# Kernel tuning notes

Measured on AMD Instinct MI355X. Metric: run time of the kernel, lower is better.

The kernel has to match this reference:

```python
import jax, jax.numpy as jnp
import numpy as np

H = 64      # hidden_dimension
NH = 4      # num_heads
L = 2       # num_egat_layers
N = 20000   # total nodes in batched graph
E = 320000  # total edges
B = 64      # number of graphs in batch
SLOPE = 0.2 # DGL EGATConv leaky_relu negative slope


def setup_inputs() -> dict:
    key = jax.random.key(0)
    ks = iter(jax.random.split(key, 40))
    def nrm(shape, scale=0.05):
        return jax.random.normal(next(ks), shape, dtype=jnp.float32) * scale
    node_graph_id = jnp.sort(jax.random.randint(next(ks), (N,), 0, B))
    src = jax.random.randint(next(ks), (E,), 0, N)
    dst = jax.random.randint(next(ks), (E,), 0, N)
    edge_graph_id = node_graph_id[dst]
    return dict(
        x=nrm((N, 81), 1.0), e=nrm((E, 17), 1.0),
        placed_rc=jax.random.randint(next(ks), (N,), 0, 2),
        fp=nrm((B, 2048), 1.0),
        src=src, dst=dst, node_graph_id=node_graph_id, edge_graph_id=edge_graph_id,
        W_fp=nrm((2048, H)), b_fp=jnp.zeros((H,), jnp.float32),
        W_n0=nrm((81, H)), b_n0=jnp.zeros((H,), jnp.float32),
        W_e0=nrm((17, H)), b_e0=jnp.zeros((H,), jnp.float32),
        emb_rc=nrm((2, H)),
        fc_node_W=nrm((L, H, NH * H)), fc_ni_W=nrm((L, H, NH * H)),
        fc_nj_W=nrm((L, H, NH * H)), fc_fij_W=nrm((L, H, NH * H)),
        attn=nrm((L, NH, H)), egat_bias=jnp.zeros((L, NH * H), jnp.float32),
        mlp_n_W=nrm((L, NH * H, H)), mlp_n_b=jnp.zeros((L, H), jnp.float32),
        mlp_e_W=nrm((L, NH * H, H)), mlp_e_b=jnp.zeros((L, H), jnp.float32),
        W_g=nrm((3 * H, H)), b_g=jnp.zeros((H,), jnp.float32),
    )


def _egat_layer(nf, ef, src, dst, p):
    # One EGATLayer: DGL EGATConv + per-output MLP + ELU.
    fcnW, fniW, fnjW, ffW, attn, ebias, mnW, mnb, meW, meb = p
    f_out = nf[src] @ fniW + nf[dst] @ fnjW + ef @ ffW          # [E, NH*H]
    f_out = jax.nn.leaky_relu(f_out, SLOPE).reshape(E, NH, H)    # [E, NH, H]
    logits = jnp.einsum('ehd,hd->eh', f_out, attn)               # [E, NH]
    # edge softmax over incoming edges at each destination node
    m = jax.ops.segment_max(logits, dst, num_segments=N)
    ex = jnp.exp(logits - m[dst])
    denom = jax.ops.segment_sum(ex, dst, num_segments=N)
    a = ex / denom[dst]                                          # [E, NH]
    h = (nf @ fcnW).reshape(N, NH, H)                            # [N, NH, H]
    msg = h[src] * a[..., None]                                  # [E, NH, H]
    h_out = jax.ops.segment_sum(msg, dst, num_segments=N)        # [N, NH, H]
    h_out = h_out + ebias.reshape(NH, H)[None]
    new_n = jax.nn.elu(h_out.reshape(N, NH * H) @ mnW + mnb)     # [N, H]
    new_e = jax.nn.elu(f_out.reshape(E, NH * H) @ meW + meb)     # [E, H]
    return new_n, new_e


def reference(x, e, placed_rc, fp, src, dst, node_graph_id, edge_graph_id,
              W_fp, b_fp, W_n0, b_n0, W_e0, b_e0, emb_rc,
              fc_node_W, fc_ni_W, fc_nj_W, fc_fij_W, attn, egat_bias,
              mlp_n_W, mlp_n_b, mlp_e_W, mlp_e_b, W_g, b_g):
    fp_enc = jax.nn.elu(fp @ W_fp + b_fp)                        # [B, H]
    nf = x @ W_n0 + b_n0 + emb_rc[placed_rc]                     # [N, H]
    ef = e @ W_e0 + b_e0                                         # [E, H]
    for l in range(L):  # residual EGAT stack
        rn, re = nf, ef
        nf, ef = _egat_layer(nf, ef, src, dst,
            (fc_node_W[l], fc_ni_W[l], fc_nj_W[l], fc_fij_W[l], attn[l],
             egat_bias[l], mlp_n_W[l], mlp_n_b[l], mlp_e_W[l], mlp_e_b[l]))
        nf = nf + rn
        ef = ef + re
    # mean readout per graph
    cnt_n = jax.ops.segment_sum(jnp.ones((N,), jnp.float32), node_graph_id, num_segments=B)
    cnt_e = jax.ops.segment_sum(jnp.ones((E,), jnp.float32), edge_graph_id, num_segments=B)
    g_n = jax.ops.segment_sum(nf, node_graph_id, num_segments=B) / jnp.maximum(cnt_n, 1.0)[:, None]
    g_e = jax.ops.segment_sum(ef, edge_graph_id, num_segments=B) / jnp.maximum(cnt_e, 1.0)[:, None]
    g = jnp.concatenate([g_n, g_e, fp_enc], axis=1)              # [B, 3H]
    g = jax.nn.elu(g @ W_g + b_g)                                # [B, H]
    return nf, g
```

## Files before the change

kernel.cpp:

```cpp
#include <hip/hip_runtime.h>
#include <math.h>

#define SLOPE 0.2f

typedef __attribute__((ext_vector_type(8))) short bf16x8;
typedef __attribute__((ext_vector_type(4))) float f32x4;

__device__ __forceinline__ unsigned short f2bf(float x) {
  unsigned int b = __float_as_uint(x);
  b = (b + 0x7fffu + ((b >> 16) & 1u)) >> 16;
  return (unsigned short)b;
}
__device__ __forceinline__ float bf2f(unsigned short u) {
  return __uint_as_float(((unsigned int)u) << 16);
}
__device__ __forceinline__ float elu1(float v) { return v > 0.f ? v : expm1f(v); }
__device__ __forceinline__ float lrelu(float v) { return v > 0.f ? v : SLOPE * v; }

__global__ __launch_bounds__(256) void k_zero(float* p, long n) {
  long i = (long)blockIdx.x * 256 + threadIdx.x;
  long stride = (long)gridDim.x * 256;
  for (; i < n; i += stride) p[i] = 0.f;
}

__global__ __launch_bounds__(256) void k_fp(const float* __restrict__ fp,
                                            const float* __restrict__ W,
                                            float* __restrict__ fpacc) {
  __shared__ float red[256];
  const int b = blockIdx.x >> 3;
  const int kc = blockIdx.x & 7;
  const int t = threadIdx.x, o = t & 63, kg = t >> 6;
  const int k0 = kc * 256 + kg * 64;
  const float* fpr = fp + (size_t)b * 2048 + k0;
  const float* Wp = W + (size_t)k0 * 64 + o;
  float a0 = 0.f, a1 = 0.f, a2 = 0.f, a3 = 0.f;
#pragma unroll
  for (int i = 0; i < 64; i += 4) {
    a0 += fpr[i + 0] * Wp[(i + 0) * 64];
    a1 += fpr[i + 1] * Wp[(i + 1) * 64];
    a2 += fpr[i + 2] * Wp[(i + 2) * 64];
    a3 += fpr[i + 3] * Wp[(i + 3) * 64];
  }
  red[t] = (a0 + a1) + (a2 + a3);
  __syncthreads();
  if (t < 64) {
    float v = red[t] + red[t + 64] + red[t + 128] + red[t + 192];
    atomicAdd(&fpacc[(size_t)b * 64 + t], v);
  }
}

__global__ __launch_bounds__(256) void k_nf0(const float* __restrict__ x,
                                             const float* __restrict__ W,
                                             const float* __restrict__ bias,
                                             const float* __restrict__ emb,
                                             const int* __restrict__ prc,
                                             float* __restrict__ nf, int N) {
  const int t = threadIdx.x, l = t & 63, q = t >> 6;
  const int n = blockIdx.x * 64 + l;
  const int nc = n < N ? n : N - 1;
  const int o0 = q * 16;
  const int pv = prc[nc];
  float acc[16];
#pragma unroll
  for (int i = 0; i < 16; ++i) acc[i] = bias[o0 + i] + emb[pv * 64 + o0 + i];
  for (int k = 0; k < 81; ++k) {
    float xv = x[(long)nc * 81 + k];
    float w[16];
    const float4* wp = (const float4*)(W + (long)k * 64 + o0);
    *(float4*)&w[0] = wp[0]; *(float4*)&w[4] = wp[1];
    *(float4*)&w[8] = wp[2]; *(float4*)&w[12] = wp[3];
#pragma unroll
    for (int i = 0; i < 16; ++i) acc[i] += xv * w[i];
  }
  if (n < N) {
#pragma unroll
    for (int u = 0; u < 4; ++u)
      *(float4*)(nf + (long)n * 64 + o0 + 4 * u) =
          make_float4(acc[4 * u], acc[4 * u + 1], acc[4 * u + 2], acc[4 * u + 3]);
  }
}

__global__ __launch_bounds__(256) void k_ef0(const float* __restrict__ ein,
                                             const int* __restrict__ eids,
                                             const float* __restrict__ W,
                                             const float* __restrict__ bias,
                                             float* __restrict__ efC, int E) {
  const int t = threadIdx.x, l = t & 63, q = t >> 6;
  const long i = (long)blockIdx.x * 64 + l;
  const long ic = i < E ? i : 0;
  const long e = eids[ic];
  const int o0 = q * 16;
  float acc[16];
#pragma unroll
  for (int k = 0; k < 16; ++k) acc[k] = bias[o0 + k];
  for (int k = 0; k < 17; ++k) {
    float xv = ein[e * 17 + k];
    float w[16];
    const float4* wp = (const float4*)(W + (long)k * 64 + o0);
    *(float4*)&w[0] = wp[0]; *(float4*)&w[4] = wp[1];
    *(float4*)&w[8] = wp[2]; *(float4*)&w[12] = wp[3];
#pragma unroll
    for (int u = 0; u < 16; ++u) acc[u] += xv * w[u];
  }
  if (i < E) {
#pragma unroll
    for (int u = 0; u < 4; ++u)
      *(float4*)(efC + i * 64 + o0 + 4 * u) =
          make_float4(acc[4 * u], acc[4 * u + 1], acc[4 * u + 2], acc[4 * u + 3]);
  }
}

__global__ __launch_bounds__(256) void k_hist(const int* __restrict__ dst, int* deg, int E) {
  int e = blockIdx.x * 256 + threadIdx.x;
  if (e < E) atomicAdd(&deg[dst[e]], 1);
}

__global__ __launch_bounds__(1024) void k_scan(const int* __restrict__ deg, int* rowst,
                                               int* cursor, int N, int E) {
  __shared__ int s[1024];
  const int t = threadIdx.x;
  const int CH = (N + 1023) / 1024;
  const int base = t * CH;
  int sum = 0;
  for (int i = 0; i < CH; ++i) { int n = base + i; if (n < N) sum += deg[n]; }
  s[t] = sum;
  __syncthreads();
  for (int off = 1; off < 1024; off <<= 1) {
    int v = (t >= off) ? s[t - off] : 0;
    __syncthreads();
    s[t] += v;
    __syncthreads();
  }
  int run = s[t] - sum;
  for (int i = 0; i < CH; ++i) {
    int n = base + i;
    if (n < N) { rowst[n] = run; cursor[n] = run; run += deg[n]; }
  }
  if (t == 1023) rowst[N] = E;
}

__global__ __launch_bounds__(256) void k_fill(const int* __restrict__ dst,
                                              const int* __restrict__ src,
                                              const int* __restrict__ egid,
                                              int* cursor, int* eids,
                                              int* srcC, int* dstC, int* egidC, int E) {
  int e = blockIdx.x * 256 + threadIdx.x;
  if (e < E) {
    int d = dst[e];
    int pos = atomicAdd(&cursor[d], 1);
    eids[pos] = e;
    srcC[pos] = src[e];
    dstC[pos] = d;
    egidC[pos] = egid[e];
  }
}

__global__ __launch_bounds__(256) void k_pack(const float* __restrict__ fni,
                                              const float* __restrict__ fnj,
                                              const float* __restrict__ ffij,
                                              const float* __restrict__ meW,
                                              unsigned short* __restrict__ pA,
                                              unsigned short* __restrict__ pB) {
  int t = blockIdx.x * 256 + threadIdx.x;
  if (t < 6144) {
    int lane = t & 63;
    int ks = (t >> 6) % 6;
    int nt = t / 384;
    int n = nt * 16 + (lane & 15);
    int kbase = ks * 32 + (lane >> 4) * 8;
    bf16x8 v;
#pragma unroll
    for (int j = 0; j < 8; ++j) {
      int kk = kbase + j;
      float wv = kk < 64 ? fni[kk * 256 + n]
                         : (kk < 128 ? fnj[(kk - 64) * 256 + n] : ffij[(kk - 128) * 256 + n]);
      v[j] = (short)f2bf(wv);
    }
    *(bf16x8*)(pA + (size_t)t * 8) = v;
  } else if (t < 8192) {
    int u = t - 6144;
    int lane = u & 63;
    int ks = (u >> 6) % 8;
    int nt = u / 512;
    int n = nt * 16 + (lane & 15);
    int kbase = ks * 32 + (lane >> 4) * 8;
    bf16x8 v;
#pragma unroll
    for (int j = 0; j < 8; ++j) v[j] = (short)f2bf(meW[(size_t)(kbase + j) * 64 + n]);
    *(bf16x8*)(pB + (size_t)u * 8) = v;
  }
}

__global__ __launch_bounds__(256) void k_comb(const float* __restrict__ fcn,
                                              const float* __restrict__ mnW,
                                              const float* __restrict__ mnb,
                                              const float* __restrict__ ebias,
                                              float* __restrict__ Wcomb,
                                              float* __restrict__ bprime) {
  const int b = blockIdx.x, t = threadIdx.x;
  if (b < 4) {
    const int h = b, i = t & 63, c0 = (t >> 6) * 16;
    float acc[16];
#pragma unroll
    for (int c = 0; c < 16; ++c) acc[c] = 0.f;
    for (int j = 0; j < 64; ++j) {
      float w1 = fcn[i * 256 + h * 64 + j];
      const float4* mp = (const float4*)(mnW + (size_t)(h * 64 + j) * 64 + c0);
      float mw[16];
      *(float4*)&mw[0] = mp[0]; *(float4*)&mw[4] = mp[1];
      *(float4*)&mw[8] = mp[2]; *(float4*)&mw[12] = mp[3];
#pragma unroll
      for (int c = 0; c < 16; ++c) acc[c] += w1 * mw[c];
    }
    for (int c = 0; c < 16; ++c) Wcomb[(size_t)(h * 64 + i) * 64 + c0 + c] = acc[c];
  } else {
    if (t < 64) {
      float a = mnb[t];
      for (int k = 0; k < 256; ++k) a += ebias[k] * mnW[(size_t)k * 64 + t];
      bprime[t] = a;
    }
  }
}

__global__ __launch_bounds__(256) void k_packB(const float* __restrict__ W,
                                               unsigned short* __restrict__ dst) {
  int u = blockIdx.x * 256 + threadIdx.x;
  if (u >= 2048) return;
  int lane = u & 63;
  int ks = (u >> 6) % 8;
  int nt = u / 512;
  int n = nt * 16 + (lane & 15);
  int kbase = ks * 32 + (lane >> 4) * 8;
  bf16x8 v;
#pragma unroll
  for (int j = 0; j < 8; ++j) v[j] = (short)f2bf(W[(size_t)(kbase + j) * 64 + n]);
  *(bf16x8*)(dst + (size_t)u * 8) = v;
}

__global__ __launch_bounds__(256, 4) void k_edge(const float* __restrict__ nf,
                                                 const float* __restrict__ efC,
                                                 const unsigned short* __restrict__ pA,
                                                 const unsigned short* __restrict__ pB,
                                                 const float* __restrict__ attnW,
                                                 const float* __restrict__ meb,
                                                 const int* __restrict__ srcC,
                                                 const int* __restrict__ dstC,
                                                 float* __restrict__ efo,
                                                 float* __restrict__ logitsC,
                                                 const int* __restrict__ egidC,
                                                 float* __restrict__ geOut,
                                                 float* __restrict__ ceOut, int E) {
  __shared__ __align__(16) char smem[32768 + 1024 + 512];
  float* lgx = (float*)(smem + 32768);
  int* sv = (int*)(smem + 32768 + 1024);
  int* dv = (int*)(smem + 32768 + 1024 + 256);
  const int t = threadIdx.x, l = t & 63, w = t >> 6;
  const long ebase = (long)blockIdx.x * 64;

  if (t < 64) sv[t] = srcC[min(ebase + t, (long)E - 1)];
  else if (t < 128) dv[t - 64] = dstC[min(ebase + t - 64, (long)E - 1)];
  __syncthreads();
#pragma unroll
  for (int i = 0; i < 6; ++i) {
    int c = i * 256 + t;
    int row = c / 24;
    int kc8 = c - row * 24;
    long e = ebase + row;
    if (e >= E) e = E - 1;
    int ko = (kc8 & 7) * 8;
    int seg = kc8 >> 3;
    const float* gp;
    if (seg == 0)      gp = nf + (size_t)sv[row] * 64 + ko;
    else if (seg == 1) gp = nf + (size_t)dv[row] * 64 + ko;
    else               gp = efC + (size_t)e * 64 + ko;
    float4 f0 = *(const float4*)gp;
    float4 f1 = *(const float4*)(gp + 4);
    bf16x8 v;
    v[0] = (short)f2bf(f0.x); v[1] = (short)f2bf(f0.y);
    v[2] = (short)f2bf(f0.z); v[3] = (short)f2bf(f0.w);
    v[4] = (short)f2bf(f1.x); v[5] = (short)f2bf(f1.y);
    v[6] = (short)f2bf(f1.z); v[7] = (short)f2bf(f1.w);
    *(bf16x8*)(smem + row * 384 + ((kc8 * 16) ^ ((row & 7) << 4))) = v;
  }
  __syncthreads();

  f32x4 acc[4][4];
#pragma unroll
  for (int c0 = 0; c0 < 4; ++c0)
#pragma unroll
    for (int e0 = 0; e0 < 4; ++e0) acc[c0][e0] = (f32x4){0.f, 0.f, 0.f, 0.f};

  for (int ks = 0; ks < 6; ++ks) {
    bf16x8 eb[4], wa[4];
#pragma unroll
    for (int e0 = 0; e0 < 4; ++e0) {
      int row = e0 * 16 + (l & 15);
      int kb = ks * 64 + (l >> 4) * 16;
      eb[e0] = *(const bf16x8*)(smem + row * 384 + (kb ^ ((row & 7) << 4)));
    }
#pragma unroll
    for (int c0 = 0; c0 < 4; ++c0)
      wa[c0] = *(const bf16x8*)(pA + (size_t)(((w * 4 + c0) * 6 + ks) * 64 + l) * 8);
#pragma unroll
    for (int c0 = 0; c0 < 4; ++c0)
#pragma unroll
      for (int e0 = 0; e0 < 4; ++e0)
        acc[c0][e0] = __builtin_amdgcn_mfma_f32_16x16x32_bf16(wa[c0], eb[e0], acc[c0][e0], 0, 0, 0);
  }
  __syncthreads();

  float avv[4][4];
#pragma unroll
  for (int c0 = 0; c0 < 4; ++c0) {
    float4 a4 = *(const float4*)(attnW + w * 64 + c0 * 16 + (l >> 4) * 4);
    avv[c0][0] = a4.x; avv[c0][1] = a4.y; avv[c0][2] = a4.z; avv[c0][3] = a4.w;
  }
  float lgp[4] = {0.f, 0.f, 0.f, 0.f};
#pragma unroll
  for (int e0 = 0; e0 < 4; ++e0) {
    int row = e0 * 16 + (l & 15);
#pragma unroll
    for (int c0 = 0; c0 < 4; ++c0) {
      float v0 = lrelu(acc[c0][e0][0]);
      float v1 = lrelu(acc[c0][e0][1]);
      float v2 = lrelu(acc[c0][e0][2]);
      float v3 = lrelu(acc[c0][e0][3]);
      lgp[e0] += v0 * avv[c0][0] + v1 * avv[c0][1] + v2 * avv[c0][2] + v3 * avv[c0][3];
      uint2 p;
      p.x = (unsigned)f2bf(v0) | ((unsigned)f2bf(v1) << 16);
      p.y = (unsigned)f2bf(v2) | ((unsigned)f2bf(v3) << 16);
      int colb = (w * 64 + c0 * 16 + (l >> 4) * 4) * 2;
      *(uint2*)(smem + row * 512 + (colb ^ ((row & 7) << 4))) = p;
    }
  }
#pragma unroll
  for (int e0 = 0; e0 < 4; ++e0) {
    float v = lgp[e0];
    v += __shfl_xor(v, 16);
    v += __shfl_xor(v, 32);
    if (l < 16) lgx[(e0 * 16 + l) * 4 + w] = v;
  }
  __syncthreads();

  if (t < 64) {
    long e = ebase + t;
    if (e < E) *(float4*)(logitsC + e * 4) = *(const float4*)(lgx + t * 4);
  }

  f32x4 a2[4];
#pragma unroll
  for (int e0 = 0; e0 < 4; ++e0) a2[e0] = (f32x4){0.f, 0.f, 0.f, 0.f};
  for (int ks = 0; ks < 8; ++ks) {
    bf16x8 fb[4];
#pragma unroll
    for (int e0 = 0; e0 < 4; ++e0) {
      int row = e0 * 16 + (l & 15);
      int kb = ks * 64 + (l >> 4) * 16;
      fb[e0] = *(const bf16x8*)(smem + row * 512 + (kb ^ ((row & 7) << 4)));
    }
    bf16x8 pb = *(const bf16x8*)(pB + (size_t)((w * 8 + ks) * 64 + l) * 8);
#pragma unroll
    for (int e0 = 0; e0 < 4; ++e0)
      a2[e0] = __builtin_amdgcn_mfma_f32_16x16x32_bf16(pb, fb[e0], a2[e0], 0, 0, 0);
  }
  const int cb = w * 16 + (l >> 4) * 4;
  float4 mb4 = *(const float4*)(meb + cb);
  __syncthreads();
#pragma unroll
  for (int e0 = 0; e0 < 4; ++e0) {
    int row = e0 * 16 + (l & 15);
    float4 o;
    o.x = elu1(a2[e0][0] + mb4.x);
    o.y = elu1(a2[e0][1] + mb4.y);
    o.z = elu1(a2[e0][2] + mb4.z);
    o.w = elu1(a2[e0][3] + mb4.w);
    *(float4*)(smem + (size_t)(row * 68 + cb) * 4) = o;
  }
  __syncthreads();
#pragma unroll
  for (int i = 0; i < 4; ++i) {
    int idx = i * 256 + t;
    int row = idx >> 4;
    int c4 = (idx & 15) * 4;
    long e = ebase + row;
    if (e < E) {
      float4 res = *(const float4*)(efC + e * 64 + c4);
      float4 v = *(const float4*)(smem + (size_t)(row * 68 + c4) * 4);
      v.x += res.x; v.y += res.y; v.z += res.z; v.w += res.w;
      *(float4*)(efo + e * 64 + c4) = v;
      if (geOut) *(float4*)(smem + (size_t)(row * 68 + c4) * 4) = v;
    }
  }
  if (geOut) {
    if (t < 64) sv[t] = (ebase + t < E) ? egidC[ebase + t] : -1;
    __syncthreads();
    if (t < 64) {
      int nrows = (int)min((long)64, E - ebase);
      float racc = 0.f, cnt = 0.f;
      int curg = sv[0];
      for (int r = 0; r < nrows; ++r) {
        int g = sv[r];
        if (g != curg) {
          atomicAdd(&geOut[(size_t)curg * 64 + t], racc);
          if (t == 0) atomicAdd(&ceOut[curg], cnt);
          racc = 0.f; cnt = 0.f; curg = g;
        }
        racc += *(const float*)(smem + (size_t)(r * 68 + t) * 4);
        cnt += 1.f;
      }
      if (curg >= 0) {
        atomicAdd(&geOut[(size_t)curg * 64 + t], racc);
        if (t == 0) atomicAdd(&ceOut[curg], cnt);
      }
    }
  }
}

__global__ __launch_bounds__(256) void k_node(const float* __restrict__ logitsC,
                                              const float* __restrict__ nf,
                                              const int* __restrict__ rowst,
                                              const int* __restrict__ srcC,
                                              unsigned short* __restrict__ agg, int N) {
  const int t = threadIdx.x, w = t >> 6, l = t & 63;
  const int n = blockIdx.x * 4 + w;
  if (n >= N) return;
  const int start = rowst[n];
  const int dg = rowst[n + 1] - start;
  const int h = l >> 4;
  float m0 = -INFINITY, m1 = -INFINITY, m2 = -INFINITY, m3 = -INFINITY;
  for (int base = 0; base < dg; base += 64) {
    int j = base + l;
    if (j < dg) {
      float4 lg = *(const float4*)(logitsC + (long)(start + j) * 4);
      m0 = fmaxf(m0, lg.x); m1 = fmaxf(m1, lg.y); m2 = fmaxf(m2, lg.z); m3 = fmaxf(m3, lg.w);
    }
  }
#pragma unroll
  for (int o = 1; o < 64; o <<= 1) {
    m0 = fmaxf(m0, __shfl_xor(m0, o)); m1 = fmaxf(m1, __shfl_xor(m1, o));
    m2 = fmaxf(m2, __shfl_xor(m2, o)); m3 = fmaxf(m3, __shfl_xor(m3, o));
  }
  float s0 = 0.f, s1 = 0.f, s2 = 0.f, s3 = 0.f;
  for (int base = 0; base < dg; base += 64) {
    int j = base + l;
    if (j < dg) {
      float4 lg = *(const float4*)(logitsC + (long)(start + j) * 4);
      s0 += __expf(lg.x - m0); s1 += __expf(lg.y - m1);
      s2 += __expf(lg.z - m2); s3 += __expf(lg.w - m3);
    }
  }
#pragma unroll
  for (int o = 1; o < 64; o <<= 1) {
    s0 += __shfl_xor(s0, o); s1 += __shfl_xor(s1, o);
    s2 += __shfl_xor(s2, o); s3 += __shfl_xor(s3, o);
  }
  const float msel = (h == 0) ? m0 : (h == 1) ? m1 : (h == 2) ? m2 : m3;
  const float ssel = (h == 0) ? s0 : (h == 1) ? s1 : (h == 2) ? s2 : s3;
  const float rsel = 1.f / ssel;

  const int co = (l & 15) * 4;
  float a0 = 0.f, a1 = 0.f, a2 = 0.f, a3 = 0.f;
  int j = 0;
  for (; j + 4 <= dg; j += 4) {
    int sj0 = srcC[start + j + 0];
    int sj1 = srcC[start + j + 1];
    int sj2 = srcC[start + j + 2];
    int sj3 = srcC[start + j + 3];
    float l0 = logitsC[(long)(start + j + 0) * 4 + h];
    float l1 = logitsC[(long)(start + j + 1) * 4 + h];
    float l2 = logitsC[(long)(start + j + 2) * 4 + h];
    float l3 = logitsC[(long)(start + j + 3) * 4 + h];
    float4 hv0 = *(const float4*)(nf + (long)sj0 * 64 + co);
    float4 hv1 = *(const float4*)(nf + (long)sj1 * 64 + co);
    float4 hv2 = *(const float4*)(nf + (long)sj2 * 64 + co);
    float4 hv3 = *(const float4*)(nf + (long)sj3 * 64 + co);
    float aa0 = __expf(l0 - msel) * rsel;
    float aa1 = __expf(l1 - msel) * rsel;
    float aa2 = __expf(l2 - msel) * rsel;
    float aa3 = __expf(l3 - msel) * rsel;
    a0 += aa0 * hv0.x + aa1 * hv1.x + aa2 * hv2.x + aa3 * hv3.x;
    a1 += aa0 * hv0.y + aa1 * hv1.y + aa2 * hv2.y + aa3 * hv3.y;
    a2 += aa0 * hv0.z + aa1 * hv1.z + aa2 * hv2.z + aa3 * hv3.z;
    a3 += aa0 * hv0.w + aa1 * hv1.w + aa2 * hv2.w + aa3 * hv3.w;
  }
  for (; j < dg; ++j) {
    int sj = srcC[start + j];
    float lg = logitsC[(long)(start + j) * 4 + h];
    float a = __expf(lg - msel) * rsel;
    float4 hv = *(const float4*)(nf + (long)sj * 64 + co);
    a0 += a * hv.x; a1 += a * hv.y; a2 += a * hv.z; a3 += a * hv.w;
  }
  unsigned v0 = (unsigned)f2bf(a0) | ((unsigned)f2bf(a1) << 16);
  unsigned v1 = (unsigned)f2bf(a2) | ((unsigned)f2bf(a3) << 16);
  uint2 vv; vv.x = v0; vv.y = v1;
  *(uint2*)(agg + (size_t)n * 256 + h * 64 + co) = vv;
}

__global__ __launch_bounds__(256, 4) void k_mlpn(const unsigned short* __restrict__ agg,
                                                 const unsigned short* __restrict__ pW,
                                                 const float* __restrict__ bprime,
                                                 float* __restrict__ nf,
                                                 float* __restrict__ dout,
                                                 const int* __restrict__ ngid,
                                                 float* __restrict__ gnOut,
                                                 float* __restrict__ cnOut, int N) {
  __shared__ __align__(16) char sm[64 * 512];
  __shared__ int gidL[64];
  const int t = threadIdx.x, l = t & 63, w = t >> 6;
  const int nbase = blockIdx.x * 64;
#pragma unroll
  for (int i = 0; i < 8; ++i) {
    int idx = t + 256 * i;
    int row = idx >> 5, kc = idx & 31;
    int rr = (nbase + row) < N ? (nbase + row) : (N - 1);
    uint4 v = *(const uint4*)(agg + (size_t)rr * 256 + kc * 8);
    *(uint4*)(sm + row * 512 + ((kc * 16) ^ ((row & 7) << 4))) = v;
  }
  __syncthreads();
  f32x4 acc[4];
#pragma unroll
  for (int e0 = 0; e0 < 4; ++e0) acc[e0] = (f32x4){0.f, 0.f, 0.f, 0.f};
  for (int ks = 0; ks < 8; ++ks) {
    bf16x8 a[4];
#pragma unroll
    for (int e0 = 0; e0 < 4; ++e0) {
      int row = e0 * 16 + (l & 15);
      int kb = ks * 64 + (l >> 4) * 16;
      a[e0] = *(const bf16x8*)(sm + row * 512 + (kb ^ ((row & 7) << 4)));
    }
    bf16x8 b = *(const bf16x8*)(pW + (size_t)((w * 8 + ks) * 64 + l) * 8);
#pragma unroll
    for (int e0 = 0; e0 < 4; ++e0)
      acc[e0] = __builtin_amdgcn_mfma_f32_16x16x32_bf16(b, a[e0], acc[e0], 0, 0, 0);
  }
  const int cb = w * 16 + (l >> 4) * 4;
  float4 bp4 = *(const float4*)(bprime + cb);
  __syncthreads();
#pragma unroll
  for (int e0 = 0; e0 < 4; ++e0) {
    int row = e0 * 16 + (l & 15);
    float4 o;
    o.x = elu1(acc[e0][0] + bp4.x);
    o.y = elu1(acc[e0][1] + bp4.y);
    o.z = elu1(acc[e0][2] + bp4.z);
    o.w = elu1(acc[e0][3] + bp4.w);
    *(float4*)(sm + (size_t)(row * 68 + cb) * 4) = o;
  }
  if (gnOut && t < 64) gidL[t] = (nbase + t < N) ? ngid[nbase + t] : -1;
  __syncthreads();
#pragma unroll
  for (int i = 0; i < 4; ++i) {
    int idx = i * 256 + t;
    int row = idx >> 4;
    int c4 = (idx & 15) * 4;
    int n = nbase + row;
    if (n < N) {
      float4 res = *(const float4*)(nf + (size_t)n * 64 + c4);
      float4 v = *(const float4*)(sm + (size_t)(row * 68 + c4) * 4);
      v.x += res.x; v.y += res.y; v.z += res.z; v.w += res.w;
      *(float4*)(nf + (size_t)n * 64 + c4) = v;
      if (dout) *(float4*)(dout + (size_t)n * 64 + c4) = v;
      if (gnOut) *(float4*)(sm + (size_t)(row * 68 + c4) * 4) = v;
    }
  }
  if (gnOut) {
    __syncthreads();
    if (t < 64) {
      int nrows = min(64, N - nbase);
      float racc = 0.f, cnt = 0.f;
      int curg = gidL[0];
      for (int r = 0; r < nrows; ++r) {
        int g = gidL[r];
        if (g != curg) {
          atomicAdd(&gnOut[(size_t)curg * 64 + t], racc);
          if (t == 0) atomicAdd(&cnOut[curg], cnt);
          racc = 0.f; cnt = 0.f; curg = g;
        }
        racc += *(const float*)(sm + (size_t)(r * 68 + t) * 4);
        cnt += 1.f;
      }
      if (curg >= 0) {
        atomicAdd(&gnOut[(size_t)curg * 64 + t], racc);
        if (t == 0) atomicAdd(&cnOut[curg], cnt);
      }
    }
  }
}

__global__ __launch_bounds__(64) void k_final(const float* __restrict__ gn,
                                              const float* __restrict__ ge,
                                              const float* __restrict__ cntn,
                                              const float* __restrict__ cnte,
                                              const float* __restrict__ fpacc,
                                              const float* __restrict__ bfp,
                                              const float* __restrict__ Wg,
                                              const float* __restrict__ bg,
                                              float* __restrict__ outg) {
  __shared__ float gv[192];
  const int b = blockIdx.x, l = threadIdx.x;
  const float rn = 1.f / fmaxf(cntn[b], 1.f);
  const float re = 1.f / fmaxf(cnte[b], 1.f);
  gv[l] = gn[(long)b * 64 + l] * rn;
  gv[64 + l] = ge[(long)b * 64 + l] * re;
  gv[128 + l] = elu1(fpacc[(long)b * 64 + l] + bfp[l]);
  __syncthreads();
  float acc = bg[l];
  for (int k = 0; k < 192; ++k) acc += gv[k] * Wg[(long)k * 64 + l];
  outg[(long)b * 64 + l] = elu1(acc);
}

extern "C" void kernel_launch(void* const* d_in, const int* in_sizes, int n_in,
                              void* d_out, int out_size, void* d_ws, size_t ws_size,
                              hipStream_t stream) {
  (void)n_in; (void)out_size; (void)ws_size;
  const float* x       = (const float*)d_in[0];
  const float* ein     = (const float*)d_in[1];
  const int*   prc     = (const int*)d_in[2];
  const float* fp      = (const float*)d_in[3];
  const int*   src     = (const int*)d_in[4];
  const int*   dst     = (const int*)d_in[5];
  const int*   ngid    = (const int*)d_in[6];
  const int*   egid    = (const int*)d_in[7];
  const float* W_fp    = (const float*)d_in[8];
  const float* b_fp    = (const float*)d_in[9];
  const float* W_n0    = (const float*)d_in[10];
  const float* b_n0    = (const float*)d_in[11];
  const float* W_e0    = (const float*)d_in[12];
  const float* b_e0    = (const float*)d_in[13];
  const float* emb_rc  = (const float*)d_in[14];
  const float* fc_node = (const float*)d_in[15];
  const float* fc_ni   = (const float*)d_in[16];
  const float* fc_nj   = (const float*)d_in[17];
  const float* fc_fij  = (const float*)d_in[18];
  const float* attnp   = (const float*)d_in[19];
  const float* egb     = (const float*)d_in[20];
  const float* mlp_n_W = (const float*)d_in[21];
  const float* mlp_n_b = (const float*)d_in[22];
  const float* mlp_e_W = (const float*)d_in[23];
  const float* mlp_e_b = (const float*)d_in[24];
  const float* W_g     = (const float*)d_in[25];
  const float* b_g     = (const float*)d_in[26];

  const int N = in_sizes[0] / 81;
  const int E = in_sizes[1] / 17;
  const int B = in_sizes[3] / 2048;
  float* out = (float*)d_out;

  char* ws = (char*)d_ws;
  size_t off = 0;
  auto carve = [&](size_t bytes) {
    size_t r = off;
    off = (off + bytes + 255) & ~(size_t)255;
    return r;
  };
  size_t o_nf   = carve((size_t)N * 64 * 4);
  size_t o_ef   = carve((size_t)E * 64 * 4);
  size_t o_agg  = carve((size_t)N * 256 * 2);
  size_t o_lg   = carve((size_t)E * 4 * 4);
  size_t o_pA   = carve((size_t)2 * 6144 * 8 * 2);
  size_t o_pB   = carve((size_t)2 * 2048 * 8 * 2);
  size_t o_Wc   = carve((size_t)2 * 256 * 64 * 4);
  size_t o_pW   = carve((size_t)2 * 2048 * 8 * 2);
  size_t o_bp   = carve((size_t)2 * 64 * 4);
  size_t o_gn   = carve((size_t)B * 64 * 4);
  size_t o_ge   = carve((size_t)B * 64 * 4);
  size_t o_cn   = carve((size_t)B * 4);
  size_t o_ce   = carve((size_t)B * 4);
  size_t o_fpe  = carve((size_t)B * 64 * 4);
  size_t o_deg  = carve((size_t)N * 4);
  size_t o_rs   = carve((size_t)(N + 1) * 4);
  size_t o_cur  = carve((size_t)N * 4);
  size_t o_eid  = carve((size_t)E * 4);
  size_t o_srcC = carve((size_t)E * 4);
  size_t o_dstC = carve((size_t)E * 4);
  size_t o_egC  = carve((size_t)E * 4);

  float* nf   = (float*)(ws + o_nf);
  float* efC  = (float*)(ws + o_ef);
  unsigned short* agg = (unsigned short*)(ws + o_agg);
  float* lgb  = (float*)(ws + o_lg);
  unsigned short* pA = (unsigned short*)(ws + o_pA);
  unsigned short* pB = (unsigned short*)(ws + o_pB);
  float* Wc   = (float*)(ws + o_Wc);
  unsigned short* pW = (unsigned short*)(ws + o_pW);
  float* bp   = (float*)(ws + o_bp);
  float* gn   = (float*)(ws + o_gn);
  float* ge   = (float*)(ws + o_ge);
  float* cn   = (float*)(ws + o_cn);
  float* ce   = (float*)(ws + o_ce);
  float* fpacc= (float*)(ws + o_fpe);
  int* deg    = (int*)(ws + o_deg);
  int* rowst  = (int*)(ws + o_rs);
  int* cursor = (int*)(ws + o_cur);
  int* eids   = (int*)(ws + o_eid);
  int* srcC   = (int*)(ws + o_srcC);
  int* dstC   = (int*)(ws + o_dstC);
  int* egidC  = (int*)(ws + o_egC);

  const long zero_n = (long)((o_deg + (size_t)N * 4 - o_gn) / 4);
  const int gridN64 = (N + 63) / 64;
  const int gridE64 = (E + 63) / 64;
  const int gridE256 = (E + 255) / 256;
  const int gridN4 = (N + 3) / 4;

  k_zero<<<128, 256, 0, stream>>>((float*)(ws + o_gn), zero_n);
  k_fp<<<B * 8, 256, 0, stream>>>(fp, W_fp, fpacc);
  k_nf0<<<gridN64, 256, 0, stream>>>(x, W_n0, b_n0, emb_rc, prc, nf, N);
  k_hist<<<gridE256, 256, 0, stream>>>(dst, deg, E);
  k_scan<<<1, 1024, 0, stream>>>(deg, rowst, cursor, N, E);
  k_fill<<<gridE256, 256, 0, stream>>>(dst, src, egid, cursor, eids, srcC, dstC, egidC, E);
  k_ef0<<<gridE64, 256, 0, stream>>>(ein, eids, W_e0, b_e0, efC, E);

  for (int l = 0; l < 2; ++l) {
    k_pack<<<32, 256, 0, stream>>>(fc_ni + (size_t)l * 64 * 256,
                                   fc_nj + (size_t)l * 64 * 256,
                                   fc_fij + (size_t)l * 64 * 256,
                                   mlp_e_W + (size_t)l * 256 * 64,
                                   pA + (size_t)l * 6144 * 8,
                                   pB + (size_t)l * 2048 * 8);
    k_comb<<<5, 256, 0, stream>>>(fc_node + (size_t)l * 64 * 256,
                                  mlp_n_W + (size_t)l * 256 * 64,
                                  mlp_n_b + (size_t)l * 64,
                                  egb + (size_t)l * 256,
                                  Wc + (size_t)l * 256 * 64,
                                  bp + (size_t)l * 64);
    k_packB<<<8, 256, 0, stream>>>(Wc + (size_t)l * 256 * 64, pW + (size_t)l * 2048 * 8);
  }

  for (int l = 0; l < 2; ++l) {
    const float* att = attnp + (size_t)l * 4 * 64;
    const float* meb = mlp_e_b + (size_t)l * 64;

    k_edge<<<gridE64, 256, 0, stream>>>(nf, efC, pA + (size_t)l * 6144 * 8,
                                        pB + (size_t)l * 2048 * 8, att, meb,
                                        srcC, dstC, efC, lgb,
                                        egidC,
                                        (l == 1) ? ge : (float*)nullptr,
                                        (l == 1) ? ce : (float*)nullptr, E);
    k_node<<<gridN4, 256, 0, stream>>>(lgb, nf, rowst, srcC, agg, N);
    k_mlpn<<<gridN64, 256, 0, stream>>>(agg, pW + (size_t)l * 2048 * 8,
                                        bp + (size_t)l * 64, nf,
                                        (l == 1) ? out : (float*)nullptr,
                                        ngid,
                                        (l == 1) ? gn : (float*)nullptr,
                                        (l == 1) ? cn : (float*)nullptr, N);
  }

  k_final<<<B, 64, 0, stream>>>(gn, ge, cn, ce, fpacc, b_fp, W_g, b_g, out + (size_t)N * 64);
}
```

Measured before the change: 545.9 us.

## Store node and edge features as bf16 to halve gather and edge traffic

Node features gain a bf16 shadow copy, and edge features are kept only in bf16, so the edge kernel gathers bf16 directly instead of loading fp32 and converting. The node aggregation also gathers bf16 neighbour features. The final-layer edge feature write is skipped because only the readout consumes it. This cuts memory traffic in the gather-heavy kernels, at the cost of bf16 rounding on the residual edge stream and extra bf16 writes for nodes.

```diff
diff --git a/kernel.cpp b/kernel.cpp
--- a/kernel.cpp
+++ b/kernel.cpp
@@ -54,7 +54,8 @@
                                              const float* __restrict__ bias,
                                              const float* __restrict__ emb,
                                              const int* __restrict__ prc,
-                                             float* __restrict__ nf, int N) {
+                                             float* __restrict__ nf,
+                                             unsigned short* __restrict__ nfB, int N) {
   const int t = threadIdx.x, l = t & 63, q = t >> 6;
   const int n = blockIdx.x * 64 + l;
   const int nc = n < N ? n : N - 1;
@@ -77,6 +78,12 @@
     for (int u = 0; u < 4; ++u)
       *(float4*)(nf + (long)n * 64 + o0 + 4 * u) =
           make_float4(acc[4 * u], acc[4 * u + 1], acc[4 * u + 2], acc[4 * u + 3]);
+    unsigned pk[8];
+#pragma unroll
+    for (int u = 0; u < 8; ++u)
+      pk[u] = (unsigned)f2bf(acc[2 * u]) | ((unsigned)f2bf(acc[2 * u + 1]) << 16);
+    *(uint4*)(nfB + (size_t)n * 64 + o0) = make_uint4(pk[0], pk[1], pk[2], pk[3]);
+    *(uint4*)(nfB + (size_t)n * 64 + o0 + 8) = make_uint4(pk[4], pk[5], pk[6], pk[7]);
   }
 }
 
@@ -84,7 +91,7 @@
                                              const int* __restrict__ eids,
                                              const float* __restrict__ W,
                                              const float* __restrict__ bias,
-                                             float* __restrict__ efC, int E) {
+                                             unsigned short* __restrict__ efB, int E) {
   const int t = threadIdx.x, l = t & 63, q = t >> 6;
   const long i = (long)blockIdx.x * 64 + l;
   const long ic = i < E ? i : 0;
@@ -103,10 +110,12 @@
     for (int u = 0; u < 16; ++u) acc[u] += xv * w[u];
   }
   if (i < E) {
-#pragma unroll
-    for (int u = 0; u < 4; ++u)
-      *(float4*)(efC + i * 64 + o0 + 4 * u) =
-          make_float4(acc[4 * u], acc[4 * u + 1], acc[4 * u + 2], acc[4 * u + 3]);
+    unsigned pk[8];
+#pragma unroll
+    for (int u = 0; u < 8; ++u)
+      pk[u] = (unsigned)f2bf(acc[2 * u]) | ((unsigned)f2bf(acc[2 * u + 1]) << 16);
+    *(uint4*)(efB + i * 64 + o0) = make_uint4(pk[0], pk[1], pk[2], pk[3]);
+    *(uint4*)(efB + i * 64 + o0 + 8) = make_uint4(pk[4], pk[5], pk[6], pk[7]);
   }
 }
 
@@ -237,15 +246,15 @@
   *(bf16x8*)(dst + (size_t)u * 8) = v;
 }
 
-__global__ __launch_bounds__(256, 4) void k_edge(const float* __restrict__ nf,
-                                                 const float* __restrict__ efC,
+__global__ __launch_bounds__(256, 4) void k_edge(const unsigned short* __restrict__ nfB,
+                                                 const unsigned short* __restrict__ efB,
                                                  const unsigned short* __restrict__ pA,
                                                  const unsigned short* __restrict__ pB,
                                                  const float* __restrict__ attnW,
                                                  const float* __restrict__ meb,
                                                  const int* __restrict__ srcC,
                                                  const int* __restrict__ dstC,
-                                                 float* __restrict__ efo,
+                                                 unsigned short* __restrict__ efBout,
                                                  float* __restrict__ logitsC,
                                                  const int* __restrict__ egidC,
                                                  float* __restrict__ geOut,
@@ -269,18 +278,12 @@
     if (e >= E) e = E - 1;
     int ko = (kc8 & 7) * 8;
     int seg = kc8 >> 3;
-    const float* gp;
-    if (seg == 0)      gp = nf + (size_t)sv[row] * 64 + ko;
-    else if (seg == 1) gp = nf + (size_t)dv[row] * 64 + ko;
-    else               gp = efC + (size_t)e * 64 + ko;
-    float4 f0 = *(const float4*)gp;
-    float4 f1 = *(const float4*)(gp + 4);
-    bf16x8 v;
-    v[0] = (short)f2bf(f0.x); v[1] = (short)f2bf(f0.y);
-    v[2] = (short)f2bf(f0.z); v[3] = (short)f2bf(f0.w);
-    v[4] = (short)f2bf(f1.x); v[5] = (short)f2bf(f1.y);
-    v[6] = (short)f2bf(f1.z); v[7] = (short)f2bf(f1.w);
-    *(bf16x8*)(smem + row * 384 + ((kc8 * 16) ^ ((row & 7) << 4))) = v;
+    const unsigned short* gp;
+    if (seg == 0)      gp = nfB + (size_t)sv[row] * 64 + ko;
+    else if (seg == 1) gp = nfB + (size_t)dv[row] * 64 + ko;
+    else               gp = efB + (size_t)e * 64 + ko;
+    uint4 v = *(const uint4*)gp;
+    *(uint4*)(smem + row * 384 + ((kc8 * 16) ^ ((row & 7) << 4))) = v;
   }
   __syncthreads();
 
@@ -384,10 +387,18 @@
     int c4 = (idx & 15) * 4;
     long e = ebase + row;
     if (e < E) {
-      float4 res = *(const float4*)(efC + e * 64 + c4);
+      uint2 rb = *(const uint2*)(efB + e * 64 + c4);
       float4 v = *(const float4*)(smem + (size_t)(row * 68 + c4) * 4);
-      v.x += res.x; v.y += res.y; v.z += res.z; v.w += res.w;
-      *(float4*)(efo + e * 64 + c4) = v;
+      v.x += bf2f((unsigned short)(rb.x & 0xffffu));
+      v.y += bf2f((unsigned short)(rb.x >> 16));
+      v.z += bf2f((unsigned short)(rb.y & 0xffffu));
+      v.w += bf2f((unsigned short)(rb.y >> 16));
+      if (efBout) {
+        uint2 ob;
+        ob.x = (unsigned)f2bf(v.x) | ((unsigned)f2bf(v.y) << 16);
+        ob.y = (unsigned)f2bf(v.z) | ((unsigned)f2bf(v.w) << 16);
+        *(uint2*)(efBout + e * 64 + c4) = ob;
+      }
       if (geOut) *(float4*)(smem + (size_t)(row * 68 + c4) * 4) = v;
     }
   }
@@ -417,7 +428,7 @@
 }
 
 __global__ __launch_bounds__(256) void k_node(const float* __restrict__ logitsC,
-                                              const float* __restrict__ nf,
+                                              const unsigned short* __restrict__ nfB,
                                               const int* __restrict__ rowst,
                                               const int* __restrict__ srcC,
                                               unsigned short* __restrict__ agg, int N) {
@@ -470,25 +481,32 @@
     float l1 = logitsC[(long)(start + j + 1) * 4 + h];
     float l2 = logitsC[(long)(start + j + 2) * 4 + h];
     float l3 = logitsC[(long)(start + j + 3) * 4 + h];
-    float4 hv0 = *(const float4*)(nf + (long)sj0 * 64 + co);
-    float4 hv1 = *(const float4*)(nf + (long)sj1 * 64 + co);
-    float4 hv2 = *(const float4*)(nf + (long)sj2 * 64 + co);
-    float4 hv3 = *(const float4*)(nf + (long)sj3 * 64 + co);
+    uint2 b0 = *(const uint2*)(nfB + (size_t)sj0 * 64 + co);
+    uint2 b1 = *(const uint2*)(nfB + (size_t)sj1 * 64 + co);
+    uint2 b2 = *(const uint2*)(nfB + (size_t)sj2 * 64 + co);
+    uint2 b3 = *(const uint2*)(nfB + (size_t)sj3 * 64 + co);
     float aa0 = __expf(l0 - msel) * rsel;
     float aa1 = __expf(l1 - msel) * rsel;
     float aa2 = __expf(l2 - msel) * rsel;
     float aa3 = __expf(l3 - msel) * rsel;
-    a0 += aa0 * hv0.x + aa1 * hv1.x + aa2 * hv2.x + aa3 * hv3.x;
-    a1 += aa0 * hv0.y + aa1 * hv1.y + aa2 * hv2.y + aa3 * hv3.y;
-    a2 += aa0 * hv0.z + aa1 * hv1.z + aa2 * hv2.z + aa3 * hv3.z;
-    a3 += aa0 * hv0.w + aa1 * hv1.w + aa2 * hv2.w + aa3 * hv3.w;
+    a0 += aa0 * bf2f((unsigned short)(b0.x & 0xffffu)) + aa1 * bf2f((unsigned short)(b1.x & 0xffffu))
+        + aa2 * bf2f((unsigned short)(b2.x & 0xffffu)) + aa3 * bf2f((unsigned short)(b3.x & 0xffffu));
+    a1 += aa0 * bf2f((unsigned short)(b0.x >> 16)) + aa1 * bf2f((unsigned short)(b1.x >> 16))
+        + aa2 * bf2f((unsigned short)(b2.x >> 16)) + aa3 * bf2f((unsigned short)(b3.x >> 16));
+    a2 += aa0 * bf2f((unsigned short)(b0.y & 0xffffu)) + aa1 * bf2f((unsigned short)(b1.y & 0xffffu))
+        + aa2 * bf2f((unsigned short)(b2.y & 0xffffu)) + aa3 * bf2f((unsigned short)(b3.y & 0xffffu));
+    a3 += aa0 * bf2f((unsigned short)(b0.y >> 16)) + aa1 * bf2f((unsigned short)(b1.y >> 16))
+        + aa2 * bf2f((unsigned short)(b2.y >> 16)) + aa3 * bf2f((unsigned short)(b3.y >> 16));
   }
   for (; j < dg; ++j) {
     int sj = srcC[start + j];
     float lg = logitsC[(long)(start + j) * 4 + h];
     float a = __expf(lg - msel) * rsel;
-    float4 hv = *(const float4*)(nf + (long)sj * 64 + co);
-    a0 += a * hv.x; a1 += a * hv.y; a2 += a * hv.z; a3 += a * hv.w;
+    uint2 b0 = *(const uint2*)(nfB + (size_t)sj * 64 + co);
+    a0 += a * bf2f((unsigned short)(b0.x & 0xffffu));
+    a1 += a * bf2f((unsigned short)(b0.x >> 16));
+    a2 += a * bf2f((unsigned short)(b0.y & 0xffffu));
+    a3 += a * bf2f((unsigned short)(b0.y >> 16));
   }
   unsigned v0 = (unsigned)f2bf(a0) | ((unsigned)f2bf(a1) << 16);
   unsigned v1 = (unsigned)f2bf(a2) | ((unsigned)f2bf(a3) << 16);
@@ -500,6 +518,7 @@
                                                  const unsigned short* __restrict__ pW,
                                                  const float* __restrict__ bprime,
                                                  float* __restrict__ nf,
+                                                 unsigned short* __restrict__ nfB,
                                                  float* __restrict__ dout,
                                                  const int* __restrict__ ngid,
                                                  float* __restrict__ gnOut,
@@ -559,6 +578,10 @@
       float4 v = *(const float4*)(sm + (size_t)(row * 68 + c4) * 4);
       v.x += res.x; v.y += res.y; v.z += res.z; v.w += res.w;
       *(float4*)(nf + (size_t)n * 64 + c4) = v;
+      uint2 ob;
+      ob.x = (unsigned)f2bf(v.x) | ((unsigned)f2bf(v.y) << 16);
+      ob.y = (unsigned)f2bf(v.z) | ((unsigned)f2bf(v.w) << 16);
+      *(uint2*)(nfB + (size_t)n * 64 + c4) = ob;
       if (dout) *(float4*)(dout + (size_t)n * 64 + c4) = v;
       if (gnOut) *(float4*)(sm + (size_t)(row * 68 + c4) * 4) = v;
     }
@@ -654,7 +677,8 @@
     return r;
   };
   size_t o_nf   = carve((size_t)N * 64 * 4);
-  size_t o_ef   = carve((size_t)E * 64 * 4);
+  size_t o_nfB  = carve((size_t)N * 64 * 2);
+  size_t o_efB  = carve((size_t)E * 64 * 2);
   size_t o_agg  = carve((size_t)N * 256 * 2);
   size_t o_lg   = carve((size_t)E * 4 * 4);
   size_t o_pA   = carve((size_t)2 * 6144 * 8 * 2);
@@ -676,7 +700,8 @@
   size_t o_egC  = carve((size_t)E * 4);
 
   float* nf   = (float*)(ws + o_nf);
-  float* efC  = (float*)(ws + o_ef);
+  unsigned short* nfB = (unsigned short*)(ws + o_nfB);
+  unsigned short* efB = (unsigned short*)(ws + o_efB);
   unsigned short* agg = (unsigned short*)(ws + o_agg);
   float* lgb  = (float*)(ws + o_lg);
   unsigned short* pA = (unsigned short*)(ws + o_pA);
@@ -705,11 +730,11 @@
 
   k_zero<<<128, 256, 0, stream>>>((float*)(ws + o_gn), zero_n);
   k_fp<<<B * 8, 256, 0, stream>>>(fp, W_fp, fpacc);
-  k_nf0<<<gridN64, 256, 0, stream>>>(x, W_n0, b_n0, emb_rc, prc, nf, N);
+  k_nf0<<<gridN64, 256, 0, stream>>>(x, W_n0, b_n0, emb_rc, prc, nf, nfB, N);
   k_hist<<<gridE256, 256, 0, stream>>>(dst, deg, E);
   k_scan<<<1, 1024, 0, stream>>>(deg, rowst, cursor, N, E);
   k_fill<<<gridE256, 256, 0, stream>>>(dst, src, egid, cursor, eids, srcC, dstC, egidC, E);
-  k_ef0<<<gridE64, 256, 0, stream>>>(ein, eids, W_e0, b_e0, efC, E);
+  k_ef0<<<gridE64, 256, 0, stream>>>(ein, eids, W_e0, b_e0, efB, E);
 
   for (int l = 0; l < 2; ++l) {
     k_pack<<<32, 256, 0, stream>>>(fc_ni + (size_t)l * 64 * 256,
@@ -731,15 +756,16 @@
     const float* att = attnp + (size_t)l * 4 * 64;
     const float* meb = mlp_e_b + (size_t)l * 64;
 
-    k_edge<<<gridE64, 256, 0, stream>>>(nf, efC, pA + (size_t)l * 6144 * 8,
+    k_edge<<<gridE64, 256, 0, stream>>>(nfB, efB, pA + (size_t)l * 6144 * 8,
                                         pB + (size_t)l * 2048 * 8, att, meb,
-                                        srcC, dstC, efC, lgb,
-                                        egidC,
+                                        srcC, dstC,
+                                        (l == 0) ? efB : (unsigned short*)nullptr,
+                                        lgb, egidC,
                                         (l == 1) ? ge : (float*)nullptr,
                                         (l == 1) ? ce : (float*)nullptr, E);
-    k_node<<<gridN4, 256, 0, stream>>>(lgb, nf, rowst, srcC, agg, N);
+    k_node<<<gridN4, 256, 0, stream>>>(lgb, nfB, rowst, srcC, agg, N);
     k_mlpn<<<gridN64, 256, 0, stream>>>(agg, pW + (size_t)l * 2048 * 8,
-                                        bp + (size_t)l * 64, nf,
+                                        bp + (size_t)l * 64, nf, nfB,
                                         (l == 1) ? out : (float*)nullptr,
                                         ngid,
                                         (l == 1) ? gn : (float*)nullptr,
```

Measured after the change: 505.4 us. -7.4%, faster.
